# Kernel tuning notes

Measured on AMD Instinct MI355X. Metric: run time of the kernel, lower is better.

## Reference

```python
import jax, jax.numpy as jnp
import numpy as np

N = 8192          # number of latent vectors z
M = 16384         # number of KDE sample points (multiple of N_EMB)
N_EMB = 16        # n_embeddings on the circle
Z_DIM = 2         # fixed by get_embeddings (cos/sin stack)
INIT_LOG_SIGMA = 0.0


def setup_inputs() -> dict:
    key = jax.random.key(0)
    k1, k2 = jax.random.split(key)
    z = jax.random.normal(k1, (N, Z_DIM), dtype=jnp.float32)
    eps = jax.random.normal(k2, (M // N_EMB, Z_DIM), dtype=jnp.float32)
    # get_embeddings: points on a circle of radius 4
    angles = jnp.linspace(0.0, 2.0 * np.pi, N_EMB)
    embeddings = (jnp.stack([jnp.cos(angles), jnp.sin(angles)], axis=1) * 4.0).astype(jnp.float32)
    log_sigma = jnp.full((1,), INIT_LOG_SIGMA, dtype=jnp.float32)
    temperature = jnp.full((1,), 0.5, dtype=jnp.float32)
    return {"z": z, "embeddings": embeddings, "log_sigma": log_sigma,
            "eps": eps, "temperature": temperature}


def reference(z, embeddings, log_sigma, eps, temperature):
    T = temperature[0]
    ls = log_sigma[0]
    sigma = jnp.exp(ls)
    z_dim = z.shape[1]
    n = z.shape[0]
    # mean: (n_emb, D); samples e: (n_emb * M//n_emb, D) == (M, D)
    mean = (1.0 - T) * embeddings
    e = (mean[:, None, :] + eps[None, :, :] * T).reshape(-1, z_dim)
    # squared euclidean distance (N, M) via gemm expansion (same math as ||z-e||^2)
    d = (jnp.sum(z * z, axis=1)[:, None]
         + jnp.sum(e * e, axis=1)[None, :]
         - 2.0 * (z @ e.T))
    alpha = -1.0 / (2.0 * sigma ** 2)
    lse = jax.nn.logsumexp(alpha * d, axis=0)  # reduce over N -> (M,)
    # np.log(np.e) == 1.0
    loss = (-jnp.mean(lse)
            + 0.5 * z_dim * (2.0 * ls - 1.0)
            + jnp.log(jnp.float32(n)))
    return loss
```

## Files before the change

### kernel.cpp

```cpp
#include <hip/hip_runtime.h>
#include <math.h>

#define N_TOT 8192
#define M_TOT 16384
#define EPS_N 1024
#define N_EMB 16

#define LOG2E 1.4426950408889634f
#define LN2   0.6931471805599453f
#define EXP2(x) __builtin_amdgcn_exp2f(x)
#define LOG2F_(x) __builtin_amdgcn_logf(x)

#define BLOCK 256
#define IC    128
#define NICH  (N_TOT / IC)
#define LCH   128
#define NLCH  (EPS_N / LCH)

__global__ __launch_bounds__(BLOCK) void gemm_partial_kernel(
    const float* __restrict__ z, const float* __restrict__ emb,
    const float* __restrict__ log_sigma, const float* __restrict__ eps,
    const float* __restrict__ temperature, float* __restrict__ part)
{
    __shared__ float4 rows[IC * 5];
    __shared__ float red[4][N_EMB * LCH];

    const int t  = threadIdx.x;
    const int l0 = blockIdx.x * LCH;
    const int ib = blockIdx.y;

    const float ls = log_sigma[0];
    const float T  = temperature[0];
    const float alpha = -0.5f * EXP2(LOG2E * (-2.0f * ls));
    const float La  = LOG2E * alpha;
    const float omT = 1.0f - T;

    {
        const int il = t & (IC - 1);
        const int kh = t >> 7;
        const int i  = ib * IC + il;
        const float z0 = z[2 * i], z1 = z[2 * i + 1];
        const float c  = La * (z0 * z0 + z1 * z1);
        const float b0 = -2.0f * La * z0, b1 = -2.0f * La * z1;
        float4 pa, pb;
#pragma unroll
        for (int kk = 0; kk < 4; ++kk) {
            int k = kh * 8 + kk;
            float m0 = omT * emb[2 * k], m1 = omT * emb[2 * k + 1];
            ((float*)&pa)[kk] = EXP2(c + b0 * m0 + b1 * m1);
        }
#pragma unroll
        for (int kk = 0; kk < 4; ++kk) {
            int k = kh * 8 + 4 + kk;
            float m0 = omT * emb[2 * k], m1 = omT * emb[2 * k + 1];
            ((float*)&pb)[kk] = EXP2(c + b0 * m0 + b1 * m1);
        }
        rows[il * 5 + kh * 2]     = pa;
        rows[il * 5 + kh * 2 + 1] = pb;
        if (kh == 0)
            rows[il * 5 + 4] = make_float4(T * b0, T * b1, 0.0f, 0.0f);
    }

    const int lane = t & 63;
    const int w    = t >> 6;
    const float2* eps2 = (const float2*)eps;
    const float2 ua = eps2[l0 + lane];
    const float2 ub = eps2[l0 + 64 + lane];

    __syncthreads();

    float sa[N_EMB] = {0.0f};
    float sb[N_EMB] = {0.0f};
#pragma unroll 2
    for (int n = 0; n < IC / 4; ++n) {
        const int ir = w * (IC / 4) + n;
        float4 p0 = rows[ir * 5 + 0];
        float4 p1 = rows[ir * 5 + 1];
        float4 p2 = rows[ir * 5 + 2];
        float4 p3 = rows[ir * 5 + 3];
        float4 tb = rows[ir * 5 + 4];
        float qa = EXP2(fmaf(tb.y, ua.y, tb.x * ua.x));
        float qb = EXP2(fmaf(tb.y, ub.y, tb.x * ub.x));
        float pk[16];
        *(float4*)&pk[0]  = p0; *(float4*)&pk[4]  = p1;
        *(float4*)&pk[8]  = p2; *(float4*)&pk[12] = p3;
#pragma unroll
        for (int k = 0; k < N_EMB; ++k) {
            sa[k] = fmaf(pk[k], qa, sa[k]);
            sb[k] = fmaf(pk[k], qb, sb[k]);
        }
    }

#pragma unroll
    for (int k = 0; k < N_EMB; ++k) {
        red[w][k * LCH + lane]      = sa[k];
        red[w][k * LCH + 64 + lane] = sb[k];
    }
    __syncthreads();
#pragma unroll
    for (int r = 0; r < (N_EMB * LCH) / BLOCK; ++r) {
        const int e  = t + r * BLOCK;
        const float S = red[0][e] + red[1][e] + red[2][e] + red[3][e];
        const int k  = e >> 7;
        const int lc = e & (LCH - 1);
        part[ib * M_TOT + k * EPS_N + l0 + lc] = S;
    }
}

__global__ __launch_bounds__(BLOCK) void reduce_final_kernel(
    const float* __restrict__ emb, const float* __restrict__ log_sigma,
    const float* __restrict__ eps, const float* __restrict__ temperature,
    const float* __restrict__ part, float* __restrict__ bsum,
    unsigned int* __restrict__ cnt, float* __restrict__ out)
{
    const int j = blockIdx.x * BLOCK + threadIdx.x;
    const float ls = log_sigma[0];
    const float T  = temperature[0];
    const float alpha = -0.5f * EXP2(LOG2E * (-2.0f * ls));

    float S = 0.0f;
#pragma unroll 16
    for (int ib = 0; ib < NICH; ++ib)
        S += part[ib * M_TOT + j];

    const int k = j >> 10, l = j & (EPS_N - 1);
    const float omT = 1.0f - T;
    const float e0 = omT * emb[2 * k]     + T * eps[2 * l];
    const float e1 = omT * emb[2 * k + 1] + T * eps[2 * l + 1];
    const float g  = LOG2E * alpha * (e0 * e0 + e1 * e1);

    float v = g + LOG2F_(S);

#pragma unroll
    for (int off = 32; off; off >>= 1) v += __shfl_down(v, off, 64);
    __shared__ float wsum[BLOCK / 64];
    __shared__ unsigned int sdone;
    const int lane = threadIdx.x & 63, w = threadIdx.x >> 6;
    if (lane == 0) wsum[w] = v;
    __syncthreads();

    if (threadIdx.x == 0) {
        const float b = wsum[0] + wsum[1] + wsum[2] + wsum[3];
        __hip_atomic_store(&bsum[blockIdx.x], b, __ATOMIC_RELAXED,
                           __HIP_MEMORY_SCOPE_AGENT);
        asm volatile("s_waitcnt vmcnt(0)" ::: "memory");
        const unsigned int old = __hip_atomic_fetch_add(
            &cnt[0], 1u, __ATOMIC_RELAXED, __HIP_MEMORY_SCOPE_AGENT);
        sdone = (old == (unsigned int)(M_TOT / BLOCK - 1)) ? 1u : 0u;
    }
    __syncthreads();
    if (sdone == 0u) return;

    if (threadIdx.x < 64) {
        float v2 = __hip_atomic_load(&bsum[threadIdx.x], __ATOMIC_RELAXED,
                                     __HIP_MEMORY_SCOPE_AGENT);
#pragma unroll
        for (int off = 32; off; off >>= 1) v2 += __shfl_down(v2, off, 64);
        if (threadIdx.x == 0) {
            const float sum_lse = v2 * LN2;
            out[0] = -sum_lse / (float)M_TOT + (2.0f * ls - 1.0f)
                     + 9.010913347279288f;
        }
    }
}

extern "C" void kernel_launch(void* const* d_in, const int* in_sizes, int n_in,
                              void* d_out, int out_size, void* d_ws, size_t ws_size,
                              hipStream_t stream)
{
    const float* z    = (const float*)d_in[0];
    const float* emb  = (const float*)d_in[1];
    const float* lsig = (const float*)d_in[2];
    const float* eps  = (const float*)d_in[3];
    const float* temp = (const float*)d_in[4];

    unsigned int* cnt = (unsigned int*)d_ws;
    float* bsum = (float*)d_ws + 16;
    float* part = (float*)d_ws + 128;

    hipMemsetAsync(d_ws, 0, 64, stream);

    dim3 grid1(NLCH, NICH);
    gemm_partial_kernel<<<grid1, BLOCK, 0, stream>>>(z, emb, lsig, eps, temp, part);
    reduce_final_kernel<<<M_TOT / BLOCK, BLOCK, 0, stream>>>(
        emb, lsig, eps, temp, part, bsum, cnt, (float*)d_out);
}
```

Baseline: 72.87 us.

## Retile gemm partials to four eps columns per thread and drop memset

Halves the z-chunk size and doubles the eps chunk per block, so each thread accumulates four eps columns and reuses each loaded row of exponentials across more FMAs. The counter reset moves into the first kernel, so the separate memset launch goes away. The trade-off is twice as many partial-sum rows for the reduce kernel to read, and higher register pressure from 64 accumulators.

```diff
diff --git a/kernel.cpp b/kernel.cpp
--- a/kernel.cpp
+++ b/kernel.cpp
@@ -12,22 +12,26 @@
 #define LOG2F_(x) __builtin_amdgcn_logf(x)
 
 #define BLOCK 256
-#define IC    128
+#define IC    64
 #define NICH  (N_TOT / IC)
-#define LCH   128
+#define LCH   256
 #define NLCH  (EPS_N / LCH)
 
 __global__ __launch_bounds__(BLOCK) void gemm_partial_kernel(
     const float* __restrict__ z, const float* __restrict__ emb,
     const float* __restrict__ log_sigma, const float* __restrict__ eps,
-    const float* __restrict__ temperature, float* __restrict__ part)
+    const float* __restrict__ temperature, float* __restrict__ part,
+    unsigned int* __restrict__ cnt)
 {
     __shared__ float4 rows[IC * 5];
-    __shared__ float red[4][N_EMB * LCH];
+    __shared__ float red[4][N_EMB * 128];
 
     const int t  = threadIdx.x;
     const int l0 = blockIdx.x * LCH;
     const int ib = blockIdx.y;
+
+    if (t == 0 && blockIdx.x == 0 && blockIdx.y == 0)
+        cnt[0] = 0u;
 
     const float ls = log_sigma[0];
     const float T  = temperature[0];
@@ -37,27 +41,20 @@
 
     {
         const int il = t & (IC - 1);
-        const int kh = t >> 7;
+        const int kq = t >> 6;
         const int i  = ib * IC + il;
         const float z0 = z[2 * i], z1 = z[2 * i + 1];
         const float c  = La * (z0 * z0 + z1 * z1);
         const float b0 = -2.0f * La * z0, b1 = -2.0f * La * z1;
-        float4 pa, pb;
+        float4 pa;
 #pragma unroll
         for (int kk = 0; kk < 4; ++kk) {
-            int k = kh * 8 + kk;
+            int k = kq * 4 + kk;
             float m0 = omT * emb[2 * k], m1 = omT * emb[2 * k + 1];
             ((float*)&pa)[kk] = EXP2(c + b0 * m0 + b1 * m1);
         }
-#pragma unroll
-        for (int kk = 0; kk < 4; ++kk) {
-            int k = kh * 8 + 4 + kk;
-            float m0 = omT * emb[2 * k], m1 = omT * emb[2 * k + 1];
-            ((float*)&pb)[kk] = EXP2(c + b0 * m0 + b1 * m1);
-        }
-        rows[il * 5 + kh * 2]     = pa;
-        rows[il * 5 + kh * 2 + 1] = pb;
-        if (kh == 0)
+        rows[il * 5 + kq] = pa;
+        if (kq == 0)
             rows[il * 5 + 4] = make_float4(T * b0, T * b1, 0.0f, 0.0f);
     }
 
@@ -66,11 +63,15 @@
     const float2* eps2 = (const float2*)eps;
     const float2 ua = eps2[l0 + lane];
     const float2 ub = eps2[l0 + 64 + lane];
+    const float2 uc = eps2[l0 + 128 + lane];
+    const float2 ud = eps2[l0 + 192 + lane];
 
     __syncthreads();
 
     float sa[N_EMB] = {0.0f};
     float sb[N_EMB] = {0.0f};
+    float sc_[N_EMB] = {0.0f};
+    float sd[N_EMB] = {0.0f};
 #pragma unroll 2
     for (int n = 0; n < IC / 4; ++n) {
         const int ir = w * (IC / 4) + n;
@@ -81,29 +82,48 @@
         float4 tb = rows[ir * 5 + 4];
         float qa = EXP2(fmaf(tb.y, ua.y, tb.x * ua.x));
         float qb = EXP2(fmaf(tb.y, ub.y, tb.x * ub.x));
+        float qc = EXP2(fmaf(tb.y, uc.y, tb.x * uc.x));
+        float qd = EXP2(fmaf(tb.y, ud.y, tb.x * ud.x));
         float pk[16];
         *(float4*)&pk[0]  = p0; *(float4*)&pk[4]  = p1;
         *(float4*)&pk[8]  = p2; *(float4*)&pk[12] = p3;
 #pragma unroll
         for (int k = 0; k < N_EMB; ++k) {
-            sa[k] = fmaf(pk[k], qa, sa[k]);
-            sb[k] = fmaf(pk[k], qb, sb[k]);
+            sa[k]  = fmaf(pk[k], qa, sa[k]);
+            sb[k]  = fmaf(pk[k], qb, sb[k]);
+            sc_[k] = fmaf(pk[k], qc, sc_[k]);
+            sd[k]  = fmaf(pk[k], qd, sd[k]);
         }
     }
 
 #pragma unroll
     for (int k = 0; k < N_EMB; ++k) {
-        red[w][k * LCH + lane]      = sa[k];
-        red[w][k * LCH + 64 + lane] = sb[k];
-    }
-    __syncthreads();
-#pragma unroll
-    for (int r = 0; r < (N_EMB * LCH) / BLOCK; ++r) {
+        red[w][k * 128 + lane]      = sa[k];
+        red[w][k * 128 + 64 + lane] = sb[k];
+    }
+    __syncthreads();
+#pragma unroll
+    for (int r = 0; r < (N_EMB * 128) / BLOCK; ++r) {
         const int e  = t + r * BLOCK;
         const float S = red[0][e] + red[1][e] + red[2][e] + red[3][e];
         const int k  = e >> 7;
-        const int lc = e & (LCH - 1);
-        part[ib * M_TOT + k * EPS_N + l0 + lc] = S;
+        const int ll = e & 127;
+        part[ib * M_TOT + k * EPS_N + l0 + ll] = S;
+    }
+    __syncthreads();
+#pragma unroll
+    for (int k = 0; k < N_EMB; ++k) {
+        red[w][k * 128 + lane]      = sc_[k];
+        red[w][k * 128 + 64 + lane] = sd[k];
+    }
+    __syncthreads();
+#pragma unroll
+    for (int r = 0; r < (N_EMB * 128) / BLOCK; ++r) {
+        const int e  = t + r * BLOCK;
+        const float S = red[0][e] + red[1][e] + red[2][e] + red[3][e];
+        const int k  = e >> 7;
+        const int ll = e & 127;
+        part[ib * M_TOT + k * EPS_N + l0 + 128 + ll] = S;
     }
 }
 
@@ -178,10 +198,9 @@
     float* bsum = (float*)d_ws + 16;
     float* part = (float*)d_ws + 128;
 
-    hipMemsetAsync(d_ws, 0, 64, stream);
-
     dim3 grid1(NLCH, NICH);
-    gemm_partial_kernel<<<grid1, BLOCK, 0, stream>>>(z, emb, lsig, eps, temp, part);
+    gemm_partial_kernel<<<grid1, BLOCK, 0, stream>>>(z, emb, lsig, eps, temp,
+                                                     part, cnt);
     reduce_final_kernel<<<M_TOT / BLOCK, BLOCK, 0, stream>>>(
         emb, lsig, eps, temp, part, bsum, cnt, (float*)d_out);
 }
```

Result: slower. 75.64 us (+3.8%).
